# Kernel tuning notes

Measured on AMD Instinct MI355X. Metric: run time of the kernel, lower is better.

## Reference

```python
import jax, jax.numpy as jnp
import numpy as np

TOKENS = 16384
IN_F = 2048
OUT_F = 2048
RANK = 32
GROUP = 64          # int4 scale group size
PAD = 256           # token padding multiple used by the fused activation quantizer
QMAX = 7.0          # signed int4 symmetric quantization


def setup_inputs() -> dict:
    key = jax.random.key(0)
    ks = jax.random.split(key, 7)
    x = jax.random.normal(ks[0], (TOKENS, IN_F), dtype=jnp.float32)
    # packed int4 weights: two signed nibbles per int8 lane
    qweight = jax.random.randint(ks[1], (OUT_F, IN_F // 2), -128, 128, dtype=jnp.int8)
    # per-group weight scales [in//group, out], strictly positive
    wscales = jnp.abs(jax.random.normal(ks[2], (IN_F // GROUP, OUT_F), dtype=jnp.float32)) * 0.01 + 1e-4
    # activation smoothing factors, positive and near 1
    smooth_factor = jnp.abs(jax.random.normal(ks[3], (IN_F,), dtype=jnp.float32)) * 0.5 + 0.75
    bias = jax.random.normal(ks[4], (OUT_F,), dtype=jnp.float32) * 0.01
    proj_down = jax.random.normal(ks[5], (IN_F, RANK), dtype=jnp.float32) * 0.02
    proj_up = jax.random.normal(ks[6], (OUT_F, RANK), dtype=jnp.float32) * 0.02
    return {"x": x, "qweight": qweight, "wscales": wscales,
            "smooth_factor": smooth_factor, "bias": bias,
            "proj_down": proj_down, "proj_up": proj_up}


def _unpack_int4(qweight):
    # low nibble = even input channel, high nibble = odd input channel; arithmetic shifts keep sign
    low = jnp.right_shift(jnp.left_shift(qweight, 4), 4)
    high = jnpp = jnp.right_shift(qweight, 4)
    w = jnp.stack([low, high], axis=-1).reshape(qweight.shape[0], qweight.shape[1] * 2)
    return w.astype(jnp.float32)  # [out, in], values in [-8, 7]


def _forward(x, qweight, wscales, smooth_factor, bias, proj_down, proj_up):
    T = x.shape[0]
    t_pad = ((T + PAD - 1) // PAD) * PAD
    # activation smoothing
    xs = x / smooth_factor
    xs_p = jnp.pad(xs, ((0, t_pad - T), (0, 0)))
    # per-token per-64-group symmetric int4 activation quantization
    xg = xs_p.reshape(t_pad, IN_F // GROUP, GROUP)
    amax = jnp.max(jnp.abs(xg), axis=-1)                       # [Tp, G]
    ascales = jnp.where(amax > 0, amax / QMAX, jnp.float32(1.0))
    qx = jnp.clip(jnp.round(xg / ascales[..., None]), -8.0, 7.0)
    xdq = (qx * ascales[..., None]).reshape(t_pad, IN_F)       # dequantized activations
    # dequantize packed int4 weights with per-group scales
    w = _unpack_int4(qweight)                                  # [out, in]
    wdq = (w.reshape(OUT_F, IN_F // GROUP, GROUP) * wscales.T[:, :, None]).reshape(OUT_F, IN_F)
    # packed GEMM (dequantized equivalent) + fused low-rank residual + bias
    y = xdq @ wdq.T                                            # [Tp, out]
    y = y + (xs_p @ proj_down) @ proj_up.T + bias
    return y[:T]


def reference(x, qweight, wscales, smooth_factor, bias, proj_down, proj_up):
    return _forward(x, qweight, wscales, smooth_factor, bias, proj_down, proj_up)
```

## Files before the change

kernel.cpp:

```cpp
#include <hip/hip_runtime.h>

#define TOKENS 16384
#define THALF 8192
#define INF 2048
#define OUTF 2048
#define RANK 32
#define BM 256
#define BN 256
#define NPER 32

typedef int   int32x4  __attribute__((ext_vector_type(4)));
typedef int   int32x2  __attribute__((ext_vector_type(2)));
typedef float floatx4  __attribute__((ext_vector_type(4)));
typedef short bf16x8   __attribute__((ext_vector_type(8)));
typedef _Float16 f16x8 __attribute__((ext_vector_type(8)));

typedef __attribute__((address_space(1))) const void gconst_t;
typedef __attribute__((address_space(3))) void ldsv_t;

__device__ __forceinline__ void gload_lds16(const void* g, void* l) {
  __builtin_amdgcn_global_load_lds((gconst_t*)g, (ldsv_t*)l, 16, 0, 0);
}

__device__ __forceinline__ unsigned short f2bf(float f) {
  unsigned u = __float_as_uint(f);
  unsigned r = (u + 0x7FFFu + ((u >> 16) & 1u)) >> 16;
  return (unsigned short)r;
}

__global__ __launch_bounds__(256) void unpack_kernel(const int* __restrict__ qw,
                                                     const float* __restrict__ wsc,
                                                     _Float16* __restrict__ wdq) {
  int idx = blockIdx.x * 256 + threadIdx.x;
  int o = idx >> 6;
  int ch = idx & 63;
  float ws = wsc[(size_t)(ch >> 1) * OUTF + o];
  const int4* src = (const int4*)qw + (size_t)idx * 4;
  _Float16* dst = wdq + (size_t)o * INF + ch * 32;
#pragma unroll
  for (int q = 0; q < 4; ++q) {
    int4 v = src[q];
    int e[4] = {v.x, v.y, v.z, v.w};
    alignas(16) _Float16 h[8];
#pragma unroll
    for (int j = 0; j < 4; ++j) {
      int lo = ((int)((unsigned)e[j] << 28)) >> 28;
      int hi = ((int)((unsigned)e[j] << 24)) >> 28;
      h[2 * j]     = (_Float16)((float)lo * ws);
      h[2 * j + 1] = (_Float16)((float)hi * ws);
    }
    *(int4*)(dst + q * 8) = *(const int4*)h;
  }
}

__global__ __launch_bounds__(256) void prep_pdT(const float* __restrict__ pd,
                                                unsigned short* __restrict__ pdT) {
  int idx = blockIdx.x * 256 + threadIdx.x;
  int r = idx >> 11, c = idx & 2047;
  pdT[idx] = f2bf(pd[(size_t)c * RANK + r]);
}

__global__ __launch_bounds__(256) void quant_kernel(
    const float* __restrict__ x, const float* __restrict__ smooth,
    const unsigned short* __restrict__ pdT,
    _Float16* __restrict__ xdq, float* __restrict__ tdown, int tbase) {
  __shared__ char lds[32768];
  int tid = threadIdx.x, lane = tid & 63, wid = tid >> 6;
  int t0rel = blockIdx.x * 32;
  int mi = wid >> 1, ni = wid & 1;
  floatx4 acc = {0.f, 0.f, 0.f, 0.f};

  floatx4 xv[8];
  floatx4 sm;
  int32x4 pv[4];

  auto issue_loads = [&](int kc) {
    const float* xb = x + (size_t)(tbase + t0rel + wid * 8) * INF + kc * 256 + lane * 4;
#pragma unroll
    for (int r = 0; r < 8; ++r) xv[r] = *(const floatx4*)(xb + r * INF);
    sm = *(const floatx4*)(smooth + kc * 256 + lane * 4);
#pragma unroll
    for (int q = 0; q < 4; ++q) {
      int flat = tid + q * 256;
      int row = flat >> 5, c16 = flat & 31;
      pv[q] = *(const int32x4*)((const char*)pdT + (size_t)row * 4096 + kc * 512 + c16 * 16);
    }
  };

  issue_loads(0);

  for (int kc = 0; kc < 8; ++kc) {
    floatx4 rsm;
    rsm[0] = 1.0f / sm[0]; rsm[1] = 1.0f / sm[1];
    rsm[2] = 1.0f / sm[2]; rsm[3] = 1.0f / sm[3];
#pragma unroll
    for (int q = 0; q < 4; ++q) {
      int flat = tid + q * 256;
      int row = flat >> 5, c16 = flat & 31;
      int byte = (row * 512 + c16 * 16) ^ ((row & 7) << 4);
      *(int32x4*)(lds + 16384 + byte) = pv[q];
    }
#pragma unroll
    for (int r = 0; r < 8; ++r) {
      floatx4 xs;
      xs[0] = xv[r][0] * rsm[0]; xs[1] = xv[r][1] * rsm[1];
      xs[2] = xv[r][2] * rsm[2]; xs[3] = xv[r][3] * rsm[3];
      float m4 = fmaxf(fmaxf(fabsf(xs[0]), fabsf(xs[1])),
                       fmaxf(fabsf(xs[2]), fabsf(xs[3])));
      m4 = fmaxf(m4, __shfl_xor(m4, 1, 64));
      m4 = fmaxf(m4, __shfl_xor(m4, 2, 64));
      m4 = fmaxf(m4, __shfl_xor(m4, 4, 64));
      m4 = fmaxf(m4, __shfl_xor(m4, 8, 64));
      float ascale = m4 > 0.f ? m4 / 7.0f : 1.0f;
      float rq = 1.0f / ascale;
      int tokrel = t0rel + wid * 8 + r;
      alignas(8) _Float16 hq[4];
#pragma unroll
      for (int b = 0; b < 4; ++b) {
        float qf = fminf(7.f, fmaxf(-8.f, rintf(xs[b] * rq)));
        hq[b] = (_Float16)(qf * ascale);
      }
      *(int32x2*)((char*)xdq + ((size_t)tokrel * INF + kc * 256 + lane * 4) * 2) =
          *(const int32x2*)hq;
      unsigned lo = (unsigned)f2bf(xs[0]) | ((unsigned)f2bf(xs[1]) << 16);
      unsigned hi = (unsigned)f2bf(xs[2]) | ((unsigned)f2bf(xs[3]) << 16);
      int lrow = wid * 8 + r;
      int xbyte = (lrow * 512 + lane * 8) ^ ((lrow & 7) << 4);
      int32x2 wv; wv[0] = (int)lo; wv[1] = (int)hi;
      *(int32x2*)(lds + xbyte) = wv;
    }
    __syncthreads();
    if (kc + 1 < 8) issue_loads(kc + 1);
#pragma unroll
    for (int ks = 0; ks < 8; ++ks) {
      int arow = mi * 16 + (lane & 15);
      int ab = (arow * 512 + ks * 64 + ((lane >> 4) << 4)) ^ ((arow & 7) << 4);
      bf16x8 av = *(const bf16x8*)(lds + ab);
      int brow = ni * 16 + (lane & 15);
      int bb = (brow * 512 + ks * 64 + ((lane >> 4) << 4)) ^ ((brow & 7) << 4);
      bf16x8 bv = *(const bf16x8*)(lds + 16384 + bb);
      acc = __builtin_amdgcn_mfma_f32_16x16x32_bf16(av, bv, acc, 0, 0, 0);
    }
    __syncthreads();
  }

  int trow = tbase + t0rel + mi * 16 + ((lane >> 4) << 2);
  int col = ni * 16 + (lane & 15);
#pragma unroll
  for (int r = 0; r < 4; ++r)
    tdown[(size_t)(trow + r) * RANK + col] = acc[r];
}

__global__ __launch_bounds__(512, 2) void gemm_kernel(
    const _Float16* __restrict__ xdq, const _Float16* __restrict__ wdq,
    const float* __restrict__ tdown, const float* __restrict__ pu,
    const float* __restrict__ bias, float* __restrict__ y,
    int tbase, int mPanels) {
  __shared__ char smem[131072];

  int tid = threadIdx.x;
  int lane = tid & 63;
  int wid = tid >> 6;
  int wm = wid >> 2, wn = wid & 3;

  int s = blockIdx.x;
  int xcd = s & 7, idx = s >> 3;
  int npan = ((xcd & 3) << 1) + (idx & 1);
  int mpan = (xcd >> 2) * (mPanels >> 1) + (idx >> 1);
  int o0 = npan * BN;
  int t0rel = mpan * BM;
  int t0abs = tbase + t0rel;

  floatx4 acc[8][4];
#pragma unroll
  for (int m = 0; m < 8; ++m)
#pragma unroll
    for (int n = 0; n < 4; ++n) acc[m][n] = (floatx4){0.f, 0.f, 0.f, 0.f};

  auto stageA = [&](int g, int h) {
    int dst = (g & 1) * 65536 + h * 16384;
#pragma unroll
    for (int i = 0; i < 2; ++i) {
      int f = i * 512 + tid;
      int row = f >> 3, sl = (f & 7) ^ (row & 7);
      gload_lds16((const char*)xdq + (size_t)(t0rel + h * 128 + row) * (INF * 2) + g * 128 + sl * 16,
                  smem + dst + i * 8192 + wid * 1024);
    }
  };
  auto stageB = [&](int g, int h) {
    int dst = (g & 1) * 65536 + 32768 + h * 16384;
#pragma unroll
    for (int i = 0; i < 2; ++i) {
      int f = i * 512 + tid;
      int row = f >> 3, sl = (f & 7) ^ (row & 7);
      gload_lds16((const char*)wdq + (size_t)(o0 + h * 128 + row) * (INF * 2) + g * 128 + sl * 16,
                  smem + dst + i * 8192 + wid * 1024);
    }
  };

  int l = lane & 15;
  int abase[2], bbase[2];
#pragma unroll
  for (int ks = 0; ks < 2; ++ks) {
    abase[ks] = wm * 16384 + l * 128 + ((((ks << 2) + (lane >> 4)) ^ (l & 7)) << 4);
    bbase[ks] = 32768 + (wn >> 1) * 16384 + ((wn & 1) * 64 + l) * 128 +
                ((((ks << 2) + (lane >> 4)) ^ (l & 7)) << 4);
  }

  stageB(0, 0); stageA(0, 0); stageB(0, 1); stageA(0, 1);
  stageB(1, 0); stageA(1, 0);

  f16x8 a03[4][2], a47[4][2], breg[4][2];

  for (int t = 0; t < NPER; ++t) {
    if (t == NPER - 1) asm volatile("s_waitcnt vmcnt(0)" ::: "memory");
    else               asm volatile("s_waitcnt vmcnt(4)" ::: "memory");
    __builtin_amdgcn_s_barrier();
    __builtin_amdgcn_sched_barrier(0);

    const char* sb = smem + (t & 1) * 65536;
    const char* pa0 = sb + abase[0];
    const char* pa1 = sb + abase[1];
    const char* pb0 = sb + bbase[0];
    const char* pb1 = sb + bbase[1];

#pragma unroll
    for (int j = 0; j < 4; ++j) {
      a03[j][0] = *(const f16x8*)(pa0 + j * 2048);
      a03[j][1] = *(const f16x8*)(pa1 + j * 2048);
    }
#pragma unroll
    for (int nf = 0; nf < 4; ++nf) {
      breg[nf][0] = *(const f16x8*)(pb0 + nf * 2048);
      breg[nf][1] = *(const f16x8*)(pb1 + nf * 2048);
    }
    if (t + 1 < NPER) { stageB(t + 1, 1); stageA(t + 1, 1); }
#pragma unroll
    for (int j = 0; j < 4; ++j) {
      a47[j][0] = *(const f16x8*)(pa0 + (4 + j) * 2048);
      a47[j][1] = *(const f16x8*)(pa1 + (4 + j) * 2048);
    }
    asm volatile("s_waitcnt lgkmcnt(8)" ::: "memory");
    __builtin_amdgcn_sched_barrier(0);
    __builtin_amdgcn_s_setprio(1);
#pragma unroll
    for (int j = 0; j < 4; ++j)
#pragma unroll
      for (int nf = 0; nf < 4; ++nf) {
        acc[j][nf] = __builtin_amdgcn_mfma_f32_16x16x32_f16(a03[j][0], breg[nf][0], acc[j][nf], 0, 0, 0);
        acc[j][nf] = __builtin_amdgcn_mfma_f32_16x16x32_f16(a03[j][1], breg[nf][1], acc[j][nf], 0, 0, 0);
      }
    __builtin_amdgcn_s_setprio(0);
    asm volatile("s_waitcnt lgkmcnt(0)" ::: "memory");
    __builtin_amdgcn_s_barrier();
    __builtin_amdgcn_sched_barrier(0);
    if (t + 2 < NPER) { stageB(t + 2, 0); stageA(t + 2, 0); }
    __builtin_amdgcn_s_setprio(1);
#pragma unroll
    for (int j = 0; j < 4; ++j)
#pragma unroll
      for (int nf = 0; nf < 4; ++nf) {
        acc[4 + j][nf] = __builtin_amdgcn_mfma_f32_16x16x32_f16(a47[j][0], breg[nf][0], acc[4 + j][nf], 0, 0, 0);
        acc[4 + j][nf] = __builtin_amdgcn_mfma_f32_16x16x32_f16(a47[j][1], breg[nf][1], acc[4 + j][nf], 0, 0, 0);
      }
    __builtin_amdgcn_s_setprio(0);
  }

  __syncthreads();

  unsigned short* td_lds = (unsigned short*)smem;
  unsigned short* pu_lds = (unsigned short*)(smem + 16384);
  {
    int row = tid >> 1, h = (tid & 1) * 16;
    const float* ts = tdown + (size_t)(t0abs + row) * RANK + h;
    const float* ps = pu + (size_t)(o0 + row) * RANK + h;
    unsigned tw[8], pw[8];
#pragma unroll
    for (int q = 0; q < 4; ++q) {
      float4 v = *(const float4*)(ts + q * 4);
      tw[q * 2 + 0] = (unsigned)f2bf(v.x) | ((unsigned)f2bf(v.y) << 16);
      tw[q * 2 + 1] = (unsigned)f2bf(v.z) | ((unsigned)f2bf(v.w) << 16);
      float4 p = *(const float4*)(ps + q * 4);
      pw[q * 2 + 0] = (unsigned)f2bf(p.x) | ((unsigned)f2bf(p.y) << 16);
      pw[q * 2 + 1] = (unsigned)f2bf(p.z) | ((unsigned)f2bf(p.w) << 16);
    }
    int4 s0, s1;
    s0.x = (int)tw[0]; s0.y = (int)tw[1]; s0.z = (int)tw[2]; s0.w = (int)tw[3];
    s1.x = (int)tw[4]; s1.y = (int)tw[5]; s1.z = (int)tw[6]; s1.w = (int)tw[7];
    *(int4*)(td_lds + row * 32 + h) = s0;
    *(int4*)(td_lds + row * 32 + h + 8) = s1;
    s0.x = (int)pw[0]; s0.y = (int)pw[1]; s0.z = (int)pw[2]; s0.w = (int)pw[3];
    s1.x = (int)pw[4]; s1.y = (int)pw[5]; s1.z = (int)pw[6]; s1.w = (int)pw[7];
    *(int4*)(pu_lds + row * 32 + h) = s0;
    *(int4*)(pu_lds + row * 32 + h + 8) = s1;
  }
  __syncthreads();

  bf16x8 ta[8], pb4[4];
  int koff8 = (lane >> 4) << 3;
#pragma unroll
  for (int m = 0; m < 8; ++m)
    ta[m] = *(const bf16x8*)&td_lds[((wm << 7) + (m << 4) + (lane & 15)) * 32 + koff8];
#pragma unroll
  for (int n = 0; n < 4; ++n)
    pb4[n] = *(const bf16x8*)&pu_lds[((wn << 6) + (n << 4) + (lane & 15)) * 32 + koff8];

#pragma unroll
  for (int n = 0; n < 4; ++n) {
    int oc = o0 + (wn << 6) + (n << 4) + (lane & 15);
    float bv = bias[oc];
#pragma unroll
    for (int m = 0; m < 8; ++m) {
      floatx4 c = acc[m][n];
      c = __builtin_amdgcn_mfma_f32_16x16x32_bf16(ta[m], pb4[n], c, 0, 0, 0);
#pragma unroll
      for (int r = 0; r < 4; ++r) {
        int tr = t0abs + (wm << 7) + (m << 4) + ((lane >> 4) << 2) + r;
        y[(size_t)tr * OUTF + oc] = c[r] + bv;
      }
    }
  }
}

extern "C" void kernel_launch(void* const* d_in, const int* in_sizes, int n_in,
                              void* d_out, int out_size, void* d_ws, size_t ws_size,
                              hipStream_t stream) {
  const float* x      = (const float*)d_in[0];
  const int*   qw     = (const int*)d_in[1];
  const float* wsc    = (const float*)d_in[2];
  const float* smooth = (const float*)d_in[3];
  const float* bias   = (const float*)d_in[4];
  const float* pd     = (const float*)d_in[5];
  const float* pu     = (const float*)d_in[6];
  float* y = (float*)d_out;

  char* ws = (char*)d_ws;
  unsigned short* pdT = (unsigned short*)((char*)d_out + (64u << 20));

  if (ws_size >= 77594624ULL) {
    _Float16* xdq = (_Float16*)ws;
    _Float16* wdq = (_Float16*)(ws + 67108864);
    float* tdown  = (float*)(ws + 67108864 + 8388608);
    unpack_kernel<<<512, 256, 0, stream>>>(qw, wsc, wdq);
    prep_pdT<<<256, 256, 0, stream>>>(pd, pdT);
    quant_kernel<<<TOKENS / 32, 256, 0, stream>>>(x, smooth, pdT, xdq, tdown, 0);
    gemm_kernel<<<8 * (TOKENS / BM), 512, 0, stream>>>(
        xdq, wdq, tdown, pu, bias, y, 0, TOKENS / BM);
  } else {
    _Float16* xdq = (_Float16*)ws;
    _Float16* wdq = (_Float16*)(ws + 33554432);
    float* tdown  = (float*)(ws + 33554432 + 8388608);
    unpack_kernel<<<512, 256, 0, stream>>>(qw, wsc, wdq);
    prep_pdT<<<256, 256, 0, stream>>>(pd, pdT);
    for (int c = 0; c < 2; ++c) {
      int tbase = c * THALF;
      quant_kernel<<<THALF / 32, 256, 0, stream>>>(x, smooth, pdT, xdq, tdown, tbase);
      gemm_kernel<<<8 * (THALF / BM), 512, 0, stream>>>(
          xdq, wdq, tdown, pu, bias, y, tbase, THALF / BM);
    }
  }
}
```

Measured before the change: 198.9 us.

## Load B fragments directly into registers and triple-buffer A in LDS

The weight (B) operand now goes straight from global memory into registers, double-buffered across iterations, instead of being staged through LDS. LDS holds only A tiles in a 3-stage ring, which shrinks LDS use and removes one barrier per iteration. The A fragment reads are interleaved with MFMA groups through lgkmcnt waits. The risks are higher register pressure from the doubled B register sets, and redundant global reads of B because the two wm warp rows each load the same B fragments, with no LDS sharing.

```diff
diff --git a/kernel.cpp b/kernel.cpp
--- a/kernel.cpp
+++ b/kernel.cpp
@@ -156,7 +156,7 @@
     const float* __restrict__ tdown, const float* __restrict__ pu,
     const float* __restrict__ bias, float* __restrict__ y,
     int tbase, int mPanels) {
-  __shared__ char smem[131072];
+  __shared__ char smem[98304];
 
   int tid = threadIdx.x;
   int lane = tid & 63;
@@ -177,93 +177,95 @@
 #pragma unroll
     for (int n = 0; n < 4; ++n) acc[m][n] = (floatx4){0.f, 0.f, 0.f, 0.f};
 
-  auto stageA = [&](int g, int h) {
-    int dst = (g & 1) * 65536 + h * 16384;
-#pragma unroll
-    for (int i = 0; i < 2; ++i) {
+  auto stageA = [&](int g) {
+    int bufb = (g % 3) * 32768;
+#pragma unroll
+    for (int i = 0; i < 4; ++i) {
       int f = i * 512 + tid;
       int row = f >> 3, sl = (f & 7) ^ (row & 7);
-      gload_lds16((const char*)xdq + (size_t)(t0rel + h * 128 + row) * (INF * 2) + g * 128 + sl * 16,
-                  smem + dst + i * 8192 + wid * 1024);
+      gload_lds16((const char*)xdq + (size_t)(t0rel + row) * (INF * 2) + g * 128 + sl * 16,
+                  smem + bufb + i * 8192 + wid * 1024);
     }
   };
-  auto stageB = [&](int g, int h) {
-    int dst = (g & 1) * 65536 + 32768 + h * 16384;
-#pragma unroll
-    for (int i = 0; i < 2; ++i) {
-      int f = i * 512 + tid;
-      int row = f >> 3, sl = (f & 7) ^ (row & 7);
-      gload_lds16((const char*)wdq + (size_t)(o0 + h * 128 + row) * (INF * 2) + g * 128 + sl * 16,
-                  smem + dst + i * 8192 + wid * 1024);
-    }
+
+  const char* bbase_g = (const char*)wdq +
+      (size_t)(o0 + (wn << 6) + (lane & 15)) * (INF * 2) + ((lane >> 4) << 4);
+
+  f16x8 b0[4][2], b1[4][2];
+  auto loadB = [&](int g, f16x8 (&b)[4][2]) {
+#pragma unroll
+    for (int nf = 0; nf < 4; ++nf)
+#pragma unroll
+      for (int ks = 0; ks < 2; ++ks)
+        b[nf][ks] = *(const f16x8*)(bbase_g + (size_t)nf * 65536 + g * 128 + ks * 64);
   };
 
   int l = lane & 15;
-  int abase[2], bbase[2];
-#pragma unroll
-  for (int ks = 0; ks < 2; ++ks) {
-    abase[ks] = wm * 16384 + l * 128 + ((((ks << 2) + (lane >> 4)) ^ (l & 7)) << 4);
-    bbase[ks] = 32768 + (wn >> 1) * 16384 + ((wn & 1) * 64 + l) * 128 +
-                ((((ks << 2) + (lane >> 4)) ^ (l & 7)) << 4);
-  }
-
-  stageB(0, 0); stageA(0, 0); stageB(0, 1); stageA(0, 1);
-  stageB(1, 0); stageA(1, 0);
-
-  f16x8 a03[4][2], a47[4][2], breg[4][2];
-
-  for (int t = 0; t < NPER; ++t) {
+  int abase[2];
+#pragma unroll
+  for (int ks = 0; ks < 2; ++ks)
+    abase[ks] = (wm * 128 + l) * 128 + ((((ks << 2) + (lane >> 4)) ^ (l & 7)) << 4);
+
+  loadB(0, b0);
+  __builtin_amdgcn_sched_barrier(0);
+  stageA(0);
+  stageA(1);
+
+  f16x8 ar[4][2];
+
+  auto body = [&](int t, f16x8 (&bcur)[4][2], f16x8 (&bnext)[4][2]) {
     if (t == NPER - 1) asm volatile("s_waitcnt vmcnt(0)" ::: "memory");
     else               asm volatile("s_waitcnt vmcnt(4)" ::: "memory");
     __builtin_amdgcn_s_barrier();
     __builtin_amdgcn_sched_barrier(0);
 
-    const char* sb = smem + (t & 1) * 65536;
-    const char* pa0 = sb + abase[0];
-    const char* pa1 = sb + abase[1];
-    const char* pb0 = sb + bbase[0];
-    const char* pb1 = sb + bbase[1];
-
-#pragma unroll
-    for (int j = 0; j < 4; ++j) {
-      a03[j][0] = *(const f16x8*)(pa0 + j * 2048);
-      a03[j][1] = *(const f16x8*)(pa1 + j * 2048);
-    }
-#pragma unroll
-    for (int nf = 0; nf < 4; ++nf) {
-      breg[nf][0] = *(const f16x8*)(pb0 + nf * 2048);
-      breg[nf][1] = *(const f16x8*)(pb1 + nf * 2048);
-    }
-    if (t + 1 < NPER) { stageB(t + 1, 1); stageA(t + 1, 1); }
-#pragma unroll
-    for (int j = 0; j < 4; ++j) {
-      a47[j][0] = *(const f16x8*)(pa0 + (4 + j) * 2048);
-      a47[j][1] = *(const f16x8*)(pa1 + (4 + j) * 2048);
-    }
-    asm volatile("s_waitcnt lgkmcnt(8)" ::: "memory");
+    const char* sb = smem + (t % 3) * 32768;
+
+#pragma unroll
+    for (int jj = 0; jj < 2; ++jj) {
+      ar[jj][0] = *(const f16x8*)(sb + abase[0] + jj * 2048);
+      ar[jj][1] = *(const f16x8*)(sb + abase[1] + jj * 2048);
+    }
+    if (t + 1 < NPER) loadB(t + 1, bnext);
     __builtin_amdgcn_sched_barrier(0);
-    __builtin_amdgcn_s_setprio(1);
-#pragma unroll
-    for (int j = 0; j < 4; ++j)
-#pragma unroll
-      for (int nf = 0; nf < 4; ++nf) {
-        acc[j][nf] = __builtin_amdgcn_mfma_f32_16x16x32_f16(a03[j][0], breg[nf][0], acc[j][nf], 0, 0, 0);
-        acc[j][nf] = __builtin_amdgcn_mfma_f32_16x16x32_f16(a03[j][1], breg[nf][1], acc[j][nf], 0, 0, 0);
+    if (t + 2 < NPER) stageA(t + 2);
+    __builtin_amdgcn_sched_barrier(0);
+#pragma unroll
+    for (int jj = 0; jj < 2; ++jj) {
+      ar[2 + jj][0] = *(const f16x8*)(sb + abase[0] + (2 + jj) * 2048);
+      ar[2 + jj][1] = *(const f16x8*)(sb + abase[1] + (2 + jj) * 2048);
+    }
+
+#pragma unroll
+    for (int p = 0; p < 4; ++p) {
+      if (p < 3) asm volatile("s_waitcnt lgkmcnt(4)" ::: "memory");
+      else       asm volatile("s_waitcnt lgkmcnt(0)" ::: "memory");
+      __builtin_amdgcn_sched_barrier(0);
+      int sel = p & 1;
+      __builtin_amdgcn_s_setprio(1);
+#pragma unroll
+      for (int jj = 0; jj < 2; ++jj)
+#pragma unroll
+        for (int nf = 0; nf < 4; ++nf) {
+          acc[p * 2 + jj][nf] = __builtin_amdgcn_mfma_f32_16x16x32_f16(
+              ar[sel * 2 + jj][0], bcur[nf][0], acc[p * 2 + jj][nf], 0, 0, 0);
+          acc[p * 2 + jj][nf] = __builtin_amdgcn_mfma_f32_16x16x32_f16(
+              ar[sel * 2 + jj][1], bcur[nf][1], acc[p * 2 + jj][nf], 0, 0, 0);
+        }
+      __builtin_amdgcn_s_setprio(0);
+      if (p < 2) {
+#pragma unroll
+        for (int jj = 0; jj < 2; ++jj) {
+          ar[sel * 2 + jj][0] = *(const f16x8*)(sb + abase[0] + ((p + 2) * 2 + jj) * 2048);
+          ar[sel * 2 + jj][1] = *(const f16x8*)(sb + abase[1] + ((p + 2) * 2 + jj) * 2048);
+        }
       }
-    __builtin_amdgcn_s_setprio(0);
-    asm volatile("s_waitcnt lgkmcnt(0)" ::: "memory");
-    __builtin_amdgcn_s_barrier();
-    __builtin_amdgcn_sched_barrier(0);
-    if (t + 2 < NPER) { stageB(t + 2, 0); stageA(t + 2, 0); }
-    __builtin_amdgcn_s_setprio(1);
-#pragma unroll
-    for (int j = 0; j < 4; ++j)
-#pragma unroll
-      for (int nf = 0; nf < 4; ++nf) {
-        acc[4 + j][nf] = __builtin_amdgcn_mfma_f32_16x16x32_f16(a47[j][0], breg[nf][0], acc[4 + j][nf], 0, 0, 0);
-        acc[4 + j][nf] = __builtin_amdgcn_mfma_f32_16x16x32_f16(a47[j][1], breg[nf][1], acc[4 + j][nf], 0, 0, 0);
-      }
-    __builtin_amdgcn_s_setprio(0);
+    }
+  };
+
+  for (int i = 0; i < NPER / 2; ++i) {
+    body(2 * i, b0, b1);
+    body(2 * i + 1, b1, b0);
   }
 
   __syncthreads();
```

New measurement: 251.4 us. +26.4%, slower.
